# Optimization experiments

Measured on AMD Instinct MI355X. Metric: run time of the kernel, lower is better.

The kernel has to match this reference:

```python
import jax, jax.numpy as jnp
import numpy as np

N_NODES = 50000
NUM_FEATURE = 256
NUM_HIDDEN = 128
NUM_CLASSES = 16
N_EDGES = 1600000


def gcn_conv(x, W, b, src, dst, deg_inv_sqrt, n_nodes):
    # GCNConv: h = x @ W ; out[i] = sum_{j->i} norm_ji * h[j] + b
    # with symmetric normalization over the self-loop-augmented graph.
    h = x @ W  # [N, out_ch]
    norm = deg_inv_sqrt[src] * deg_inv_sqrt[dst]  # [E']
    msgs = h[src] * norm[:, None]  # [E', out_ch] (dominant intermediate)
    out = jax.ops.segment_sum(msgs, dst, num_segments=n_nodes)
    return out + b


def setup_inputs() -> dict:
    key = jax.random.key(0)
    k_x, k_e, k_w1, k_b1, k_w2, k_b2 = jax.random.split(key, 6)
    x = jax.random.normal(k_x, (N_NODES, NUM_FEATURE), dtype=jnp.float32)
    edge_index = jax.random.randint(k_e, (2, N_EDGES), 0, N_NODES, dtype=jnp.int64)
    # Glorot init like PyG's GCNConv linear
    s1 = (6.0 / (NUM_FEATURE + NUM_HIDDEN)) ** 0.5
    s2 = (6.0 / (NUM_HIDDEN + NUM_CLASSES)) ** 0.5
    W1 = jax.random.uniform(k_w1, (NUM_FEATURE, NUM_HIDDEN), jnp.float32, -s1, s1)
    b1 = jnp.zeros((NUM_HIDDEN,), jnp.float32)
    W2 = jax.random.uniform(k_w2, (NUM_HIDDEN, NUM_CLASSES), jnp.float32, -s2, s2)
    b2 = jnp.zeros((NUM_CLASSES,), jnp.float32)
    return {"x": x, "edge_index": edge_index, "W1": W1, "b1": b1, "W2": W2, "b2": b2}


def reference(x, edge_index, W1, b1, W2, b2):
    n = x.shape[0]
    # add self-loops (done inside GCNConv for each layer; identical both times)
    loops = jnp.arange(n, dtype=edge_index.dtype)
    src = jnp.concatenate([edge_index[0], loops])
    dst = jnp.concatenate([edge_index[1], loops])
    deg = jax.ops.segment_sum(jnp.ones_like(dst, dtype=x.dtype), dst, num_segments=n)
    deg_inv_sqrt = jnp.where(deg > 0, jax.lax.rsqrt(deg), 0.0)

    h = jax.nn.relu(gcn_conv(x, W1, b1, src, dst, deg_inv_sqrt, n))
    # F.dropout with training=False is the identity (eval-mode baseline)
    logits = gcn_conv(h, W2, b2, src, dst, deg_inv_sqrt, n)
    return jax.nn.log_softmax(logits, axis=1)
```

## Files before the change

### kernel.cpp

```cpp
#include <hip/hip_runtime.h>
#include <hip/hip_fp16.h>
#include <math.h>

#define NF 256
#define NH 128
#define NC 16
#define NB 391
#define NBLK 512

typedef __attribute__((ext_vector_type(8))) short bf16x8;
typedef __attribute__((ext_vector_type(4))) float f32x4;

__device__ __forceinline__ unsigned f2b(float f) {
    unsigned u = __float_as_uint(f);
    return (u + 0x7FFFu + ((u >> 16) & 1u)) >> 16;
}
__device__ __forceinline__ unsigned packt(float a, float b) {
    return (__float_as_uint(a) >> 16) | (__float_as_uint(b) & 0xFFFF0000u);
}

__global__ void passA_kernel(const int* __restrict__ dst, int* __restrict__ hist, int E) {
    __shared__ int h[NB];
    for (int i = threadIdx.x; i < NB; i += 256) h[i] = 0;
    __syncthreads();
    int b = blockIdx.x;
    int e0 = (int)((long long)b * E / NBLK), e1 = (int)((long long)(b + 1) * E / NBLK);
    for (int e = e0 + (int)threadIdx.x; e < e1; e += 256)
        atomicAdd(&h[dst[e] >> 7], 1);
    __syncthreads();
    for (int i = threadIdx.x; i < NB; i += 256) hist[b * NB + i] = h[i];
}

__global__ void scanR_kernel(const int* __restrict__ hist, int* __restrict__ bsum) {
    __shared__ int sm[NBLK];
    int k = blockIdx.x, t = threadIdx.x;
    sm[t] = hist[t * NB + k];
    __syncthreads();
    for (int off = NBLK / 2; off > 0; off >>= 1) {
        if (t < off) sm[t] += sm[t + off];
        __syncthreads();
    }
    if (t == 0) bsum[k] = sm[0];
}

__global__ void scanB_kernel(const int* __restrict__ bsum, int* __restrict__ ubase,
                             int* __restrict__ pbase, int N, int E) {
    __shared__ int smu[512];
    __shared__ int smp[512];
    int t = threadIdx.x;
    int vu = (t < NB) ? bsum[t] : 0;
    int vp = (t < NB) ? (((vu + 7) & ~7) + 904) : 0;
    smu[t] = vu; smp[t] = vp;
    __syncthreads();
    for (int off = 1; off < 512; off <<= 1) {
        int uu = (t >= off) ? smu[t - off] : 0;
        int pp = (t >= off) ? smp[t - off] : 0;
        __syncthreads();
        smu[t] += uu; smp[t] += pp;
        __syncthreads();
    }
    if (t < NB) { ubase[t] = smu[t] - vu; pbase[t] = smp[t] - vp; }
    if (t == 0) ubase[NB] = E;
}

__global__ void scanC_kernel(int* __restrict__ hist, const int* __restrict__ ubase) {
    __shared__ int sm[NBLK];
    int k = blockIdx.x, t = threadIdx.x;
    int v = hist[t * NB + k];
    sm[t] = v;
    __syncthreads();
    for (int off = 1; off < NBLK; off <<= 1) {
        int u = (t >= off) ? sm[t - off] : 0;
        __syncthreads();
        sm[t] += u;
        __syncthreads();
    }
    hist[t * NB + k] = ubase[k] + sm[t] - v;
}

__global__ void passB_kernel(const int* __restrict__ src, const int* __restrict__ dst,
                             const int* __restrict__ hist, unsigned* __restrict__ ebuf,
                             int E) {
    __shared__ int cur[NB];
    int b = blockIdx.x;
    for (int i = threadIdx.x; i < NB; i += 256) cur[i] = hist[b * NB + i];
    __syncthreads();
    int e0 = (int)((long long)b * E / NBLK), e1 = (int)((long long)(b + 1) * E / NBLK);
    for (int e = e0 + (int)threadIdx.x; e < e1; e += 256) {
        int d = dst[e];
        int pos = atomicAdd(&cur[d >> 7], 1);
        ebuf[pos] = ((unsigned)d << 16) | (unsigned)src[e];
    }
}

__global__ void passC_kernel(const unsigned* __restrict__ ebuf, const int* __restrict__ ubase,
                             const int* __restrict__ pbase, int* __restrict__ rowptr,
                             int* __restrict__ degs, float* __restrict__ dis,
                             unsigned short* __restrict__ colidx, int N) {
    __shared__ int h[128];
    __shared__ int s2[128];
    __shared__ int curp[128];
    int k = blockIdx.x, t = threadIdx.x;
    if (t < 128) h[t] = 0;
    __syncthreads();
    int e0 = ubase[k], e1 = ubase[k + 1];
    for (int e = e0 + t; e < e1; e += 256)
        atomicAdd(&h[(ebuf[e] >> 16) & 127], 1);
    __syncthreads();
    int v = (t < 128) ? h[t] : 0;
    int pd = (v + 7) & ~7;
    if (t < 128) s2[t] = pd;
    __syncthreads();
    for (int off = 1; off < 128; off <<= 1) {
        int u = (t < 128 && t >= off) ? s2[t - off] : 0;
        __syncthreads();
        if (t < 128) s2[t] += u;
        __syncthreads();
    }
    if (t < 128) {
        int start = pbase[k] + s2[t] - pd;
        int node = k * 128 + t;
        if (node < N) {
            rowptr[node] = start;
            degs[node] = v;
            dis[node] = rsqrtf((float)(v + 1));
        }
        curp[t] = start;
    }
    __syncthreads();
    for (int e = e0 + t; e < e1; e += 256) {
        unsigned w = ebuf[e];
        int dl = (w >> 16) & 127;
        int pos = atomicAdd(&curp[dl], 1);
        colidx[pos] = (unsigned short)(w & 0xFFFFu);
    }
    __syncthreads();
    if (t < 128) {
        int endp = pbase[k] + s2[t];
        for (int q = curp[t]; q < endp; ++q) colidx[q] = (unsigned short)N;
    }
}

__global__ void w1t_kernel(const float* __restrict__ W1, unsigned short* __restrict__ W1T,
                           unsigned* __restrict__ h1T, unsigned* __restrict__ h2sb, int N) {
    int idx = blockIdx.x * 256 + threadIdx.x;
    int n = idx >> 8, k = idx & 255;
    W1T[n * 256 + k] = (unsigned short)f2b(W1[(size_t)k * NH + n]);
    if (idx < 64) {
        int p = idx >> 4, j = idx & 15;
        h1T[(size_t)p * (N + 1) * 16 + (size_t)N * 16 + j] = 0u;
    } else if (idx < 72) {
        h2sb[(size_t)N * 8 + (idx - 64)] = 0u;
    }
}

__global__ __launch_bounds__(256, 3) void gemm1_mfma_kernel(
    const float* __restrict__ x, const unsigned short* __restrict__ W1T,
    const float* __restrict__ dis, unsigned short* __restrict__ h1us, int N) {
    int tid = threadIdx.x;
    int wid = tid >> 6, lane = tid & 63;
    int lrow = lane & 15, lk = lane >> 4;
    int rb = blockIdx.x * 64 + wid * 16;
    int ra = rb + lrow;
    int rc = ra < N ? ra : N - 1;
    const float* xr = x + (size_t)rc * NF + lk * 8;

    bf16x8 a[8];
#pragma unroll
    for (int kk = 0; kk < 8; ++kk) {
        float4 lo = *reinterpret_cast<const float4*>(xr + kk * 32);
        float4 hi = *reinterpret_cast<const float4*>(xr + kk * 32 + 4);
        union { unsigned u[4]; bf16x8 v; } av;
        av.u[0] = packt(lo.x, lo.y);
        av.u[1] = packt(lo.z, lo.w);
        av.u[2] = packt(hi.x, hi.y);
        av.u[3] = packt(hi.z, hi.w);
        a[kk] = av.v;
    }

    f32x4 acc[8];
#pragma unroll
    for (int t = 0; t < 8; ++t) acc[t] = (f32x4){0.f, 0.f, 0.f, 0.f};

    const unsigned short* wbase = W1T + (size_t)lrow * 256 + lk * 8;
#pragma unroll
    for (int nt = 0; nt < 8; ++nt) {
        const unsigned short* wp = wbase + (size_t)nt * 16 * 256;
        bf16x8 b0 = *(const bf16x8*)(wp + 0 * 32);
        bf16x8 b1 = *(const bf16x8*)(wp + 1 * 32);
        bf16x8 b2 = *(const bf16x8*)(wp + 2 * 32);
        bf16x8 b3 = *(const bf16x8*)(wp + 3 * 32);
        bf16x8 b4 = *(const bf16x8*)(wp + 4 * 32);
        bf16x8 b5 = *(const bf16x8*)(wp + 5 * 32);
        bf16x8 b6 = *(const bf16x8*)(wp + 6 * 32);
        bf16x8 b7 = *(const bf16x8*)(wp + 7 * 32);
        acc[nt] = __builtin_amdgcn_mfma_f32_16x16x32_bf16(a[0], b0, acc[nt], 0, 0, 0);
        acc[nt] = __builtin_amdgcn_mfma_f32_16x16x32_bf16(a[1], b1, acc[nt], 0, 0, 0);
        acc[nt] = __builtin_amdgcn_mfma_f32_16x16x32_bf16(a[2], b2, acc[nt], 0, 0, 0);
        acc[nt] = __builtin_amdgcn_mfma_f32_16x16x32_bf16(a[3], b3, acc[nt], 0, 0, 0);
        acc[nt] = __builtin_amdgcn_mfma_f32_16x16x32_bf16(a[4], b4, acc[nt], 0, 0, 0);
        acc[nt] = __builtin_amdgcn_mfma_f32_16x16x32_bf16(a[5], b5, acc[nt], 0, 0, 0);
        acc[nt] = __builtin_amdgcn_mfma_f32_16x16x32_bf16(a[6], b6, acc[nt], 0, 0, 0);
        acc[nt] = __builtin_amdgcn_mfma_f32_16x16x32_bf16(a[7], b7, acc[nt], 0, 0, 0);
    }

    int crow0 = rb + lk * 4;
#pragma unroll
    for (int r = 0; r < 4; ++r) {
        int row = crow0 + r;
        if (row < N) {
            float dr = dis[row];
#pragma unroll
            for (int nt = 0; nt < 8; ++nt) {
                size_t ad = ((size_t)(nt >> 1) * (N + 1) + row) * 32 + ((nt & 1) * 16 + lrow);
                __half hv = __float2half(acc[nt][r] * dr);
                h1us[ad] = __half_as_ushort(hv);
            }
        }
    }
}

__global__ __launch_bounds__(256) void aggall_kernel(
    const int* __restrict__ rowptr, const int* __restrict__ degs,
    const unsigned short* __restrict__ colidx,
    const __half2* __restrict__ h1T, __half2* __restrict__ aggT, int N, int bps) {
    int p = blockIdx.x / bps;
    int i = (blockIdx.x - p * bps) * 16 + (threadIdx.x >> 4);
    if (i >= N) return;
    int l = threadIdx.x & 15;
    const __half2* slab = h1T + (size_t)p * (N + 1) * 16;
    __half2 acc = slab[(size_t)i * 16 + l];
    int e = rowptr[i];
    int cnt8 = (degs[i] + 7) >> 3;
    if (cnt8 > 0) {
        uint4 w = *reinterpret_cast<const uint4*>(colidx + e);
        for (int b = 1; b < cnt8; ++b) {
            uint4 wn = *reinterpret_cast<const uint4*>(colidx + e + 8 * b);
            int a0 = w.x & 0xFFFF, a1 = w.x >> 16;
            int a2 = w.y & 0xFFFF, a3 = w.y >> 16;
            int a4 = w.z & 0xFFFF, a5 = w.z >> 16;
            int a6 = w.w & 0xFFFF, a7 = w.w >> 16;
            __half2 v0 = slab[(size_t)a0 * 16 + l];
            __half2 v1 = slab[(size_t)a1 * 16 + l];
            __half2 v2 = slab[(size_t)a2 * 16 + l];
            __half2 v3 = slab[(size_t)a3 * 16 + l];
            __half2 v4 = slab[(size_t)a4 * 16 + l];
            __half2 v5 = slab[(size_t)a5 * 16 + l];
            __half2 v6 = slab[(size_t)a6 * 16 + l];
            __half2 v7 = slab[(size_t)a7 * 16 + l];
            __half2 s01 = __hadd2(v0, v1), s23 = __hadd2(v2, v3);
            __half2 s45 = __hadd2(v4, v5), s67 = __hadd2(v6, v7);
            acc = __hadd2(acc, __hadd2(__hadd2(s01, s23), __hadd2(s45, s67)));
            w = wn;
        }
        int a0 = w.x & 0xFFFF, a1 = w.x >> 16;
        int a2 = w.y & 0xFFFF, a3 = w.y >> 16;
        int a4 = w.z & 0xFFFF, a5 = w.z >> 16;
        int a6 = w.w & 0xFFFF, a7 = w.w >> 16;
        __half2 v0 = slab[(size_t)a0 * 16 + l];
        __half2 v1 = slab[(size_t)a1 * 16 + l];
        __half2 v2 = slab[(size_t)a2 * 16 + l];
        __half2 v3 = slab[(size_t)a3 * 16 + l];
        __half2 v4 = slab[(size_t)a4 * 16 + l];
        __half2 v5 = slab[(size_t)a5 * 16 + l];
        __half2 v6 = slab[(size_t)a6 * 16 + l];
        __half2 v7 = slab[(size_t)a7 * 16 + l];
        __half2 s01 = __hadd2(v0, v1), s23 = __hadd2(v2, v3);
        __half2 s45 = __hadd2(v4, v5), s67 = __hadd2(v6, v7);
        acc = __hadd2(acc, __hadd2(__hadd2(s01, s23), __hadd2(s45, s67)));
    }
    aggT[(size_t)p * N * 16 + (size_t)i * 16 + l] = acc;
}

__global__ __launch_bounds__(256) void relu_gemm2_kernel(
    const __half2* __restrict__ aggT, const float* __restrict__ dis,
    const float* __restrict__ b1, const float* __restrict__ W2,
    __half2* __restrict__ h2sb, int N) {
    __shared__ float sW2[NH * NC];
    __shared__ float srow[4][NH];
    int tid = threadIdx.x;
    for (int k = tid; k < NH * NC; k += 256) sW2[k] = W2[k];
    __syncthreads();

    int wid = tid >> 6, lane = tid & 63;
    int i = blockIdx.x * 4 + wid;
    if (i >= N) return;
    int p = lane >> 4, l16 = lane & 15;
    float2 f = __half22float2(aggT[((size_t)p * N + i) * 16 + l16]);
    float di = dis[i];
    int c0 = p * 32 + l16 * 2;
    srow[wid][c0]     = fmaxf(di * f.x + b1[c0], 0.f);
    srow[wid][c0 + 1] = fmaxf(di * f.y + b1[c0 + 1], 0.f);
    int j = lane & 15, q = lane >> 4;
    const float* rw = srow[wid];
    float pacc = 0.f;
#pragma unroll
    for (int cc = 0; cc < 32; ++cc) {
        int c = q * 32 + cc;
        pacc += rw[c] * sW2[c * NC + j];
    }
    pacc += __shfl_xor(pacc, 16, 64);
    pacc += __shfl_xor(pacc, 32, 64);
    float dp = di * pacc;
    float plo = __shfl(dp, (lane << 1) & 63, 64);
    float phi = __shfl(dp, ((lane << 1) | 1) & 63, 64);
    if (lane < 8) h2sb[(size_t)i * 8 + lane] = __floats2half2_rn(plo, phi);
}

__global__ void layer2_kernel(const int* __restrict__ rowptr, const int* __restrict__ degs,
                              const unsigned short* __restrict__ colidx,
                              const __half2* __restrict__ h2sb, const float* __restrict__ dis,
                              const float* __restrict__ b2, float* __restrict__ out, int N) {
    int t = blockIdx.x * 256 + threadIdx.x;
    int i = t >> 3;
    if (i >= N) return;
    int j2 = t & 7;
    int e = rowptr[i];
    int cnt4 = (degs[i] + 3) >> 2;
    __half2 acc = h2sb[(size_t)i * 8 + j2];
    if (cnt4 > 0) {
        uint2 w = *reinterpret_cast<const uint2*>(colidx + e);
        for (int b = 1; b < cnt4; ++b) {
            uint2 wn = *reinterpret_cast<const uint2*>(colidx + e + 4 * b);
            int a0 = w.x & 0xFFFF, a1 = w.x >> 16;
            int a2 = w.y & 0xFFFF, a3 = w.y >> 16;
            __half2 g0 = h2sb[(size_t)a0 * 8 + j2];
            __half2 g1 = h2sb[(size_t)a1 * 8 + j2];
            __half2 g2 = h2sb[(size_t)a2 * 8 + j2];
            __half2 g3 = h2sb[(size_t)a3 * 8 + j2];
            acc = __hadd2(acc, __hadd2(__hadd2(g0, g1), __hadd2(g2, g3)));
            w = wn;
        }
        int a0 = w.x & 0xFFFF, a1 = w.x >> 16;
        int a2 = w.y & 0xFFFF, a3 = w.y >> 16;
        __half2 g0 = h2sb[(size_t)a0 * 8 + j2];
        __half2 g1 = h2sb[(size_t)a1 * 8 + j2];
        __half2 g2 = h2sb[(size_t)a2 * 8 + j2];
        __half2 g3 = h2sb[(size_t)a3 * 8 + j2];
        acc = __hadd2(acc, __hadd2(__hadd2(g0, g1), __hadd2(g2, g3)));
    }
    float2 f = __half22float2(acc);
    float di = dis[i];
    float l0 = di * f.x + b2[2 * j2];
    float l1 = di * f.y + b2[2 * j2 + 1];
    float m = fmaxf(l0, l1);
    m = fmaxf(m, __shfl_xor(m, 1, 64));
    m = fmaxf(m, __shfl_xor(m, 2, 64));
    m = fmaxf(m, __shfl_xor(m, 4, 64));
    float s = __expf(l0 - m) + __expf(l1 - m);
    s += __shfl_xor(s, 1, 64);
    s += __shfl_xor(s, 2, 64);
    s += __shfl_xor(s, 4, 64);
    float lse = m + __logf(s);
    float2 o = make_float2(l0 - lse, l1 - lse);
    *reinterpret_cast<float2*>(out + (size_t)i * NC + 2 * j2) = o;
}

extern "C" void kernel_launch(void* const* d_in, const int* in_sizes, int n_in,
                              void* d_out, int out_size, void* d_ws, size_t ws_size,
                              hipStream_t stream) {
    const float* x  = (const float*)d_in[0];
    const int*   ei = (const int*)d_in[1];
    const float* W1 = (const float*)d_in[2];
    const float* b1 = (const float*)d_in[3];
    const float* W2 = (const float*)d_in[4];
    const float* b2 = (const float*)d_in[5];
    float* out = (float*)d_out;

    const int N = in_sizes[0] / NF;
    const int E = in_sizes[1] / 2;
    const int* src = ei;
    const int* dst = ei + E;

    __half2*        h1T    = (__half2*)d_ws;
    __half2*        aggT   = h1T + (size_t)4 * (N + 1) * 16;
    __half2*        h2sb   = aggT + (size_t)4 * N * 16;
    float*          dis    = (float*)(h2sb + (size_t)(N + 1) * 8);
    int*            degs   = (int*)(dis + N);
    int*            rowptr = degs + N;
    int*            hist   = rowptr + N;
    int*            bsum   = hist + NBLK * NB;
    int*            ubase  = bsum + NB;
    int*            pbase  = ubase + NB + 1;
    unsigned*       ebuf   = (unsigned*)(pbase + NB + 1);
    unsigned short* colidx = (unsigned short*)(ebuf + E);
    unsigned short* W1T    = (unsigned short*)ebuf;

    passA_kernel<<<NBLK, 256, 0, stream>>>(dst, hist, E);
    scanR_kernel<<<NB, NBLK, 0, stream>>>(hist, bsum);
    scanB_kernel<<<1, 512, 0, stream>>>(bsum, ubase, pbase, N, E);
    scanC_kernel<<<NB, NBLK, 0, stream>>>(hist, ubase);
    passB_kernel<<<NBLK, 256, 0, stream>>>(src, dst, hist, ebuf, E);
    passC_kernel<<<NB, 256, 0, stream>>>(ebuf, ubase, pbase, rowptr, degs, dis, colidx, N);

    w1t_kernel<<<128, 256, 0, stream>>>(W1, W1T, (unsigned*)h1T, (unsigned*)h2sb, N);

    gemm1_mfma_kernel<<<(N + 63) / 64, 256, 0, stream>>>(x, W1T, dis,
                                                         (unsigned short*)h1T, N);

    const int bps = (N + 15) / 16;
    aggall_kernel<<<4 * bps, 256, 0, stream>>>(rowptr, degs, colidx, h1T, aggT, N, bps);

    relu_gemm2_kernel<<<(N + 3) / 4, 256, 0, stream>>>(aggT, dis, b1, W2, h2sb, N);

    layer2_kernel<<<((size_t)N * 8 + 255) / 256, 256, 0, stream>>>(rowptr, degs, colidx, h2sb, dis, b2, out, N);
}
```

Before: 167.6 us.

## Stage x tiles into LDS via direct global-to-LDS loads and use nontemporal accesses

The first-layer GEMM now copies each block's 64 rows of x into a 64KB XOR-swizzled shared-memory tile with global_load_lds, then reads the A fragments from LDS instead of straight from global memory. Its occupancy bound drops from 3 to 2 blocks per CU to make room for the shared tile. Separately, several streaming accesses become nontemporal loads and stores: the column-index reads in both aggregation kernels, and the h1, aggregate and output writes. The aim is to cut uncoalesced global reads in the GEMM and keep streamed data from evicting the gathered feature rows from cache, at the cost of lower occupancy and an extra barrier.

Result: slower. 188.0 us (+12.1%).

```diff
diff --git a/kernel.cpp b/kernel.cpp
--- a/kernel.cpp
+++ b/kernel.cpp
@@ -10,6 +10,9 @@
 
 typedef __attribute__((ext_vector_type(8))) short bf16x8;
 typedef __attribute__((ext_vector_type(4))) float f32x4;
+typedef unsigned u32x4 __attribute__((ext_vector_type(4)));
+typedef unsigned u32x2 __attribute__((ext_vector_type(2)));
+typedef float f32x2 __attribute__((ext_vector_type(2)));
 
 __device__ __forceinline__ unsigned f2b(float f) {
     unsigned u = __float_as_uint(f);
@@ -18,6 +21,7 @@
 __device__ __forceinline__ unsigned packt(float a, float b) {
     return (__float_as_uint(a) >> 16) | (__float_as_uint(b) & 0xFFFF0000u);
 }
+union h2u { __half2 h; unsigned u; };
 
 __global__ void passA_kernel(const int* __restrict__ dst, int* __restrict__ hist, int E) {
     __shared__ int h[NB];
@@ -154,33 +158,49 @@
     }
 }
 
-__global__ __launch_bounds__(256, 3) void gemm1_mfma_kernel(
+__global__ __launch_bounds__(256, 2) void gemm1_mfma_kernel(
     const float* __restrict__ x, const unsigned short* __restrict__ W1T,
     const float* __restrict__ dis, unsigned short* __restrict__ h1us, int N) {
+    __shared__ char sx[65536];
     int tid = threadIdx.x;
     int wid = tid >> 6, lane = tid & 63;
+
+    {
+        int fsw = (wid & 3) << 1;
+        for (int it = 0; it < 16; ++it) {
+            int lr = it * 4 + wid;
+            int grow = blockIdx.x * 64 + lr;
+            if (grow >= N) grow = N - 1;
+            const char* gp = (const char*)x + (size_t)grow * 1024 + ((lane ^ fsw) << 4);
+            __builtin_amdgcn_global_load_lds(gp, sx + it * 4096 + wid * 1024 + lane * 16,
+                                             16, 0, 0);
+        }
+    }
+    __syncthreads();
+
     int lrow = lane & 15, lk = lane >> 4;
     int rb = blockIdx.x * 64 + wid * 16;
-    int ra = rb + lrow;
-    int rc = ra < N ? ra : N - 1;
-    const float* xr = x + (size_t)rc * NF + lk * 8;
+    int lr = wid * 16 + lrow;
+    int fr = (lrow & 3) << 1;
+    const float4* lds4 = (const float4*)sx;
+
+    f32x4 acc[8];
+#pragma unroll
+    for (int t = 0; t < 8; ++t) acc[t] = (f32x4){0.f, 0.f, 0.f, 0.f};
 
     bf16x8 a[8];
 #pragma unroll
     for (int kk = 0; kk < 8; ++kk) {
-        float4 lo = *reinterpret_cast<const float4*>(xr + kk * 32);
-        float4 hi = *reinterpret_cast<const float4*>(xr + kk * 32 + 4);
-        union { unsigned u[4]; bf16x8 v; } av;
+        int v = (kk * 8 + lk * 2) ^ fr;
+        float4 lo = lds4[lr * 64 + v];
+        float4 hi = lds4[lr * 64 + v + 1];
+        union { unsigned u[4]; bf16x8 vv; } av;
         av.u[0] = packt(lo.x, lo.y);
         av.u[1] = packt(lo.z, lo.w);
         av.u[2] = packt(hi.x, hi.y);
         av.u[3] = packt(hi.z, hi.w);
-        a[kk] = av.v;
-    }
-
-    f32x4 acc[8];
-#pragma unroll
-    for (int t = 0; t < 8; ++t) acc[t] = (f32x4){0.f, 0.f, 0.f, 0.f};
+        a[kk] = av.vv;
+    }
 
     const unsigned short* wbase = W1T + (size_t)lrow * 256 + lk * 8;
 #pragma unroll
@@ -214,7 +234,7 @@
             for (int nt = 0; nt < 8; ++nt) {
                 size_t ad = ((size_t)(nt >> 1) * (N + 1) + row) * 32 + ((nt & 1) * 16 + lrow);
                 __half hv = __float2half(acc[nt][r] * dr);
-                h1us[ad] = __half_as_ushort(hv);
+                __builtin_nontemporal_store(__half_as_ushort(hv), &h1us[ad]);
             }
         }
     }
@@ -233,9 +253,9 @@
     int e = rowptr[i];
     int cnt8 = (degs[i] + 7) >> 3;
     if (cnt8 > 0) {
-        uint4 w = *reinterpret_cast<const uint4*>(colidx + e);
+        u32x4 w = __builtin_nontemporal_load((const u32x4*)(colidx + e));
         for (int b = 1; b < cnt8; ++b) {
-            uint4 wn = *reinterpret_cast<const uint4*>(colidx + e + 8 * b);
+            u32x4 wn = __builtin_nontemporal_load((const u32x4*)(colidx + e + 8 * b));
             int a0 = w.x & 0xFFFF, a1 = w.x >> 16;
             int a2 = w.y & 0xFFFF, a3 = w.y >> 16;
             int a4 = w.z & 0xFFFF, a5 = w.z >> 16;
@@ -269,7 +289,8 @@
         __half2 s45 = __hadd2(v4, v5), s67 = __hadd2(v6, v7);
         acc = __hadd2(acc, __hadd2(__hadd2(s01, s23), __hadd2(s45, s67)));
     }
-    aggT[(size_t)p * N * 16 + (size_t)i * 16 + l] = acc;
+    h2u cu; cu.h = acc;
+    __builtin_nontemporal_store(cu.u, (unsigned*)&aggT[(size_t)p * N * 16 + (size_t)i * 16 + l]);
 }
 
 __global__ __launch_bounds__(256) void relu_gemm2_kernel(
@@ -286,7 +307,9 @@
     int i = blockIdx.x * 4 + wid;
     if (i >= N) return;
     int p = lane >> 4, l16 = lane & 15;
-    float2 f = __half22float2(aggT[((size_t)p * N + i) * 16 + l16]);
+    h2u cu;
+    cu.u = __builtin_nontemporal_load((const unsigned*)&aggT[((size_t)p * N + i) * 16 + l16]);
+    float2 f = __half22float2(cu.h);
     float di = dis[i];
     int c0 = p * 32 + l16 * 2;
     srow[wid][c0]     = fmaxf(di * f.x + b1[c0], 0.f);
@@ -319,9 +342,9 @@
     int cnt4 = (degs[i] + 3) >> 2;
     __half2 acc = h2sb[(size_t)i * 8 + j2];
     if (cnt4 > 0) {
-        uint2 w = *reinterpret_cast<const uint2*>(colidx + e);
+        u32x2 w = __builtin_nontemporal_load((const u32x2*)(colidx + e));
         for (int b = 1; b < cnt4; ++b) {
-            uint2 wn = *reinterpret_cast<const uint2*>(colidx + e + 4 * b);
+            u32x2 wn = __builtin_nontemporal_load((const u32x2*)(colidx + e + 4 * b));
             int a0 = w.x & 0xFFFF, a1 = w.x >> 16;
             int a2 = w.y & 0xFFFF, a3 = w.y >> 16;
             __half2 g0 = h2sb[(size_t)a0 * 8 + j2];
@@ -352,8 +375,9 @@
     s += __shfl_xor(s, 2, 64);
     s += __shfl_xor(s, 4, 64);
     float lse = m + __logf(s);
-    float2 o = make_float2(l0 - lse, l1 - lse);
-    *reinterpret_cast<float2*>(out + (size_t)i * NC + 2 * j2) = o;
+    f32x2 o;
+    o.x = l0 - lse; o.y = l1 - lse;
+    __builtin_nontemporal_store(o, (f32x2*)(out + (size_t)i * NC + 2 * j2));
 }
 
 extern "C" void kernel_launch(void* const* d_in, const int* in_sizes, int n_in,
```
